# Optimization experiments

Hardware: AMD Instinct MI355X
Metric: run time of the kernel (lower is better)

Reference implementation:

```python
import math
import jax, jax.numpy as jnp
import numpy as np

S = 32.0
M1 = 1.0
M2 = 0.5
M3 = 0.0
MM = M2 * math.sin(math.pi - M2)
NUM_CLASSES = 100000
FEATURES = 512
BATCH = 512


def setup_inputs() -> dict:
    key = jax.random.key(0)
    k1, k2, k3 = jax.random.split(key, 3)
    inputs = jax.random.normal(k1, (BATCH, FEATURES), dtype=jnp.float32)
    labels = jax.random.randint(k2, (BATCH,), 0, NUM_CLASSES, dtype=jnp.int64)
    # xavier_uniform on [num_classes, features]
    limit = math.sqrt(6.0 / (NUM_CLASSES + FEATURES))
    weight = jax.random.uniform(k3, (NUM_CLASSES, FEATURES), minval=-limit, maxval=limit, dtype=jnp.float32)
    return {"inputs": inputs, "labels": labels, "weight": weight}


def reference(inputs, labels, weight):
    # L2 normalize (torch F.normalize uses eps=1e-12 clamp on norm)
    inp_n = inputs / jnp.maximum(jnp.linalg.norm(inputs, axis=1, keepdims=True), 1e-12)
    w_n = weight / jnp.maximum(jnp.linalg.norm(weight, axis=1, keepdims=True), 1e-12)
    cos_in = jnp.clip(inp_n @ w_n.T, -1.0 + 1e-6, 1.0 - 1e-6)  # [N, C]
    theta_in = jnp.arccos(cos_in)
    one_hot = jax.nn.one_hot(labels, NUM_CLASSES, dtype=cos_in.dtype)
    theta_out = theta_in + (theta_in * (M1 - 1.0) + M2) * one_hot
    cos_out = jnp.where(
        theta_out < math.pi,
        jnp.cos(theta_out) - M3 * one_hot,
        cos_in - MM * one_hot - M3 * one_hot,
    )
    outs = S * cos_out  # [N, C]
    # mean cross-entropy
    logp = jax.nn.log_softmax(outs, axis=1)
    n = jnp.arange(BATCH)
    loss = -jnp.mean(logp[n, labels])
    target_cos_in = cos_in[n, labels][:, None]
    target_theta_in = theta_in[n, labels][:, None]
    target_cos_out = cos_out[n, labels][:, None]
    return loss, outs, target_cos_in, target_theta_in, target_cos_out
```

## Files before the change

kernel.cpp:

```cpp
#include <hip/hip_runtime.h>
#include <stdint.h>

#define BATCH 512
#define FEAT 512
#define NCLS 100000
#define BM 128
#define BN 128
#define BK 64
#define NBLK_N 782
#define NBLK (NBLK_N * 4)
#define NCHUNK (NBLK_N * 2)
#define SCALE_S 32.0f
#define MARGIN 0.5f
#define MM_CONST 0.23971276930210156f
#define PI_F 3.14159265358979f

typedef unsigned int u32;
typedef unsigned short u16;
typedef __bf16 bf16x8 __attribute__((ext_vector_type(8)));
typedef float f32x4 __attribute__((ext_vector_type(4)));

__device__ __forceinline__ u16 f2bf(float f) {
  u32 u = __float_as_uint(f);
  u += 0x7fffu + ((u >> 16) & 1u);
  return (u16)(u >> 16);
}

__device__ __forceinline__ void async_copy16(const void* g, void* l) {
  __builtin_amdgcn_global_load_lds((const __attribute__((address_space(1))) u32*)g,
                                   (__attribute__((address_space(3))) u32*)l,
                                   16, 0, 0);
}

__device__ __forceinline__ float block_reduce_sum(float v, float* sbuf) {
  for (int off = 1; off < 64; off <<= 1) v += __shfl_xor(v, off, 64);
  int wid = threadIdx.x >> 6, lane = threadIdx.x & 63;
  __syncthreads();
  if (lane == 0) sbuf[wid] = v;
  __syncthreads();
  return sbuf[0] + sbuf[1] + sbuf[2] + sbuf[3];
}

__global__ __launch_bounds__(256) void norm_all_kernel(const float* __restrict__ inputs,
                                                       const float* __restrict__ weight,
                                                       u16* __restrict__ dstA,
                                                       u16* __restrict__ dstB,
                                                       float* __restrict__ out0) {
  if (blockIdx.x == 0 && threadIdx.x == 0) out0[0] = 0.0f;
  const int lane = threadIdx.x & 63;
  const int gw = (blockIdx.x * 256 + threadIdx.x) >> 6;
  const int nw = gridDim.x * 4;
  for (int row = gw; row < BATCH + NCLS; row += nw) {
    const float* src;
    u16* dst;
    if (row < BATCH) {
      src = inputs + (size_t)row * FEAT;
      dst = dstA + (size_t)row * FEAT;
    } else {
      src = weight + (size_t)(row - BATCH) * FEAT;
      dst = dstB + (size_t)(row - BATCH) * FEAT;
    }
    const float4* p4 = (const float4*)src;
    float4 a = p4[lane];
    float4 b = p4[lane + 64];
    float ss = a.x * a.x + a.y * a.y + a.z * a.z + a.w * a.w +
               b.x * b.x + b.y * b.y + b.z * b.z + b.w * b.w;
#pragma unroll
    for (int off = 1; off < 64; off <<= 1) ss += __shfl_xor(ss, off, 64);
    float inv = 1.0f / fmaxf(sqrtf(ss), 1e-12f);
    ushort4 oa, ob;
    oa.x = f2bf(a.x * inv); oa.y = f2bf(a.y * inv);
    oa.z = f2bf(a.z * inv); oa.w = f2bf(a.w * inv);
    ob.x = f2bf(b.x * inv); ob.y = f2bf(b.y * inv);
    ob.z = f2bf(b.z * inv); ob.w = f2bf(b.w * inv);
    ((ushort4*)dst)[lane] = oa;
    ((ushort4*)dst)[lane + 64] = ob;
  }
}

__global__ __launch_bounds__(256, 3) void gemm_kernel(const u16* __restrict__ A,
                                                      const u16* __restrict__ B,
                                                      const int* __restrict__ labels,
                                                      float* __restrict__ outs,
                                                      float* __restrict__ partials) {
  __shared__ __align__(16) u16 sB0[BN * BK];
  __shared__ __align__(16) u16 sB1[BN * BK];
  __shared__ __align__(16) u16 sB2[BN * BK];
  __shared__ int sLab[BM];

  const int tid = threadIdx.x;
  const int lane = tid & 63;
  const int wid = tid >> 6;
  const int waveM = wid >> 1, waveN = wid & 1;
  const int orig = blockIdx.x;
  const int L = (orig & 7) * (NBLK / 8) + (orig >> 3);
  const int bm = L & 3, bn = L >> 2;
  const int quad = lane >> 4, l15 = lane & 15;

  if (tid < BM) sLab[tid] = labels[bm * BM + tid];

  const u16* gB[4];
#pragma unroll
  for (int rd = 0; rd < 4; ++rd) {
    int idx = rd * 256 + tid;
    int r = idx >> 3;
    int cb = (idx & 7) ^ (r & 7);
    int brow = bn * BN + r;
    if (brow >= NCLS) brow = NCLS - 1;
    gB[rd] = B + (size_t)brow * FEAT + cb * 8;
  }
  const u16* gA = A + (size_t)(bm * BM + waveM * 64 + l15) * FEAT;

  f32x4 acc[4][4] = {};
  bf16x8 a0[4][2], a1[4][2];

#define STAGE_B(SBUF, KT)                                                   \
  do {                                                                      \
    _Pragma("unroll") for (int rd = 0; rd < 4; ++rd)                        \
        async_copy16(gB[rd] + (KT)*BK, &(SBUF)[(rd * 256 + tid) * 8]);      \
  } while (0)

#define LOAD_A(AREG, KT)                                                    \
  do {                                                                      \
    _Pragma("unroll") for (int mi = 0; mi < 4; ++mi)                        \
        _Pragma("unroll") for (int ks = 0; ks < 2; ++ks)                    \
            AREG[mi][ks] = *(const bf16x8*)(gA + (size_t)mi * 16 * FEAT +   \
                                            (KT)*BK + (ks * 4 + quad) * 8); \
  } while (0)

#define COMPUTE(SBUF, AREG)                                                 \
  do {                                                                      \
    _Pragma("unroll") for (int ks = 0; ks < 2; ++ks) {                      \
      int j0 = ks * 4 + quad;                                               \
      bf16x8 bF[4];                                                         \
      _Pragma("unroll") for (int ni = 0; ni < 4; ++ni) {                    \
        int r = waveN * 64 + ni * 16 + l15;                                 \
        bF[ni] = *(const bf16x8*)&(SBUF)[(r * 8 + (j0 ^ (r & 7))) * 8];     \
      }                                                                     \
      _Pragma("unroll") for (int mi = 0; mi < 4; ++mi)                      \
          _Pragma("unroll") for (int ni = 0; ni < 4; ++ni)                  \
              acc[mi][ni] = __builtin_amdgcn_mfma_f32_16x16x32_bf16(        \
                  AREG[mi][ks], bF[ni], acc[mi][ni], 0, 0, 0);              \
    }                                                                       \
  } while (0)

#define SCHED0 __builtin_amdgcn_sched_barrier(0)
#define VMCNT(N) asm volatile("s_waitcnt vmcnt(" #N ")" ::: "memory")
#define BAR asm volatile("s_barrier" ::: "memory")

  STAGE_B(sB0, 0);
  STAGE_B(sB1, 1);
  LOAD_A(a0, 0);
  __syncthreads();

  LOAD_A(a1, 1); SCHED0; STAGE_B(sB2, 2); SCHED0;
  COMPUTE(sB0, a0);
  BAR;
  LOAD_A(a0, 2); SCHED0; STAGE_B(sB0, 3); SCHED0;
  VMCNT(16);
  COMPUTE(sB1, a1);
  BAR;
  LOAD_A(a1, 3); SCHED0; STAGE_B(sB1, 4); SCHED0;
  VMCNT(16); BAR;
  COMPUTE(sB2, a0);
  BAR;
  LOAD_A(a0, 4); SCHED0; STAGE_B(sB2, 5); SCHED0;
  VMCNT(16); BAR;
  COMPUTE(sB0, a1);
  BAR;
  LOAD_A(a1, 5); SCHED0; STAGE_B(sB0, 6); SCHED0;
  VMCNT(16); BAR;
  COMPUTE(sB1, a0);
  BAR;
  LOAD_A(a0, 6); SCHED0; STAGE_B(sB1, 7); SCHED0;
  VMCNT(16); BAR;
  COMPUTE(sB2, a1);
  BAR;
  LOAD_A(a1, 7); SCHED0;
  VMCNT(12); BAR;
  COMPUTE(sB0, a0);
  BAR;
  VMCNT(0); BAR;
  COMPUTE(sB1, a1);

#undef STAGE_B
#undef LOAD_A
#undef COMPUTE

#pragma unroll
  for (int mi = 0; mi < 4; ++mi) {
#pragma unroll
    for (int reg = 0; reg < 4; ++reg) {
      int rloc = waveM * 64 + mi * 16 + quad * 4 + reg;
      int rg = bm * BM + rloc;
      int lab = sLab[rloc];
      float rsum = 0.f;
#pragma unroll
      for (int ni = 0; ni < 4; ++ni) {
        int cg = bn * BN + waveN * 64 + ni * 16 + l15;
        float v = acc[mi][ni][reg];
        v = fminf(fmaxf(v, -1.0f + 1e-6f), 1.0f - 1e-6f);
        if (cg == lab) {
          float th = acosf(v) + MARGIN;
          v = (th < PI_F) ? cosf(th) : (v - MM_CONST);
        }
        v *= SCALE_S;
        if (cg < NCLS) {
          __builtin_nontemporal_store(v, &outs[(size_t)rg * NCLS + cg]);
          rsum += __expf(v - SCALE_S);
        }
      }
#pragma unroll
      for (int off = 1; off < 16; off <<= 1) rsum += __shfl_xor(rsum, off, 64);
      if (l15 == 0) partials[(size_t)rg * NCHUNK + (bn * 2 + waveN)] = rsum;
    }
  }
}

__global__ __launch_bounds__(256) void combine_kernel(const float* __restrict__ partials,
                                                      const float* __restrict__ outs,
                                                      const int* __restrict__ labels,
                                                      const float* __restrict__ inputs,
                                                      const float* __restrict__ weight,
                                                      float* __restrict__ out0,
                                                      float* __restrict__ tdst) {
  __shared__ float sbuf[4];
  int r = blockIdx.x, tid = threadIdx.x;
  int lab = labels[r];

  const float2* px = (const float2*)(inputs + (size_t)r * FEAT);
  const float2* pw = (const float2*)(weight + (size_t)lab * FEAT);
  float2 x = px[tid], w = pw[tid];
  float dot = block_reduce_sum(x.x * w.x + x.y * w.y, sbuf);
  float sx = block_reduce_sum(x.x * x.x + x.y * x.y, sbuf);
  float sw = block_reduce_sum(w.x * w.x + w.y * w.y, sbuf);

  const float* p = partials + (size_t)r * NCHUNK;
  float l = 0.f;
  for (int i = tid; i < NCHUNK; i += 256) l += p[i];
  float lt = block_reduce_sum(l, sbuf);

  if (tid == 0) {
    float lse = SCALE_S + logf(lt);
    float tgt = outs[(size_t)r * NCLS + lab];
    atomicAdd(out0, (lse - tgt) * (1.0f / BATCH));

    float inv = 1.0f / (fmaxf(sqrtf(sx), 1e-12f) * fmaxf(sqrtf(sw), 1e-12f));
    float ci = fminf(fmaxf(dot * inv, -1.0f + 1e-6f), 1.0f - 1e-6f);
    float th = acosf(ci);
    float t2 = th + MARGIN;
    float co = (t2 < PI_F) ? cosf(t2) : (ci - MM_CONST);
    tdst[r] = ci;
    tdst[BATCH + r] = th;
    tdst[2 * BATCH + r] = co;
  }
}

extern "C" void kernel_launch(void* const* d_in, const int* in_sizes, int n_in,
                              void* d_out, int out_size, void* d_ws, size_t ws_size,
                              hipStream_t stream) {
  const float* inputs = (const float*)d_in[0];
  const int* labels = (const int*)d_in[1];
  const float* weight = (const float*)d_in[2];
  float* out = (float*)d_out;
  float* outs = out + 1;
  float* tdst = out + 1 + (size_t)BATCH * NCLS;

  char* ws = (char*)d_ws;
  u16* wsA = (u16*)ws;
  u16* wsB = (u16*)(ws + 524288);
  float* partials = (float*)(ws + 524288 + 102400000);

  norm_all_kernel<<<2048, 256, 0, stream>>>(inputs, weight, wsA, wsB, out);
  gemm_kernel<<<NBLK, 256, 0, stream>>>(wsA, wsB, labels, outs, partials);
  combine_kernel<<<BATCH, 256, 0, stream>>>(partials, outs, labels, inputs, weight, out, tdst);
}
```

Baseline: 563.4 us.

## Load full-K 64-column B tile into LDS once and stream A through registers

```diff
diff --git a/kernel.cpp b/kernel.cpp
--- a/kernel.cpp
+++ b/kernel.cpp
@@ -5,11 +5,10 @@
 #define FEAT 512
 #define NCLS 100000
 #define BM 128
-#define BN 128
-#define BK 64
-#define NBLK_N 782
-#define NBLK (NBLK_N * 4)
-#define NCHUNK (NBLK_N * 2)
+#define BN 64
+#define NBN 1563
+#define NBLK (NBN * 4)
+#define NCHUNK NBN
 #define SCALE_S 32.0f
 #define MARGIN 0.5f
 #define MM_CONST 0.23971276930210156f
@@ -78,126 +77,95 @@
   }
 }
 
-__global__ __launch_bounds__(256, 3) void gemm_kernel(const u16* __restrict__ A,
+__global__ __launch_bounds__(256, 2) void gemm_kernel(const u16* __restrict__ A,
                                                       const u16* __restrict__ B,
                                                       const int* __restrict__ labels,
                                                       float* __restrict__ outs,
                                                       float* __restrict__ partials) {
-  __shared__ __align__(16) u16 sB0[BN * BK];
-  __shared__ __align__(16) u16 sB1[BN * BK];
-  __shared__ __align__(16) u16 sB2[BN * BK];
-  __shared__ int sLab[BM];
+  __shared__ __align__(16) u16 sB[BN * FEAT];
 
   const int tid = threadIdx.x;
   const int lane = tid & 63;
-  const int wid = tid >> 6;
-  const int waveM = wid >> 1, waveN = wid & 1;
-  const int orig = blockIdx.x;
-  const int L = (orig & 7) * (NBLK / 8) + (orig >> 3);
-  const int bm = L & 3, bn = L >> 2;
+  const int w = tid >> 6;
   const int quad = lane >> 4, l15 = lane & 15;
 
-  if (tid < BM) sLab[tid] = labels[bm * BM + tid];
-
-  const u16* gB[4];
-#pragma unroll
-  for (int rd = 0; rd < 4; ++rd) {
-    int idx = rd * 256 + tid;
-    int r = idx >> 3;
-    int cb = (idx & 7) ^ (r & 7);
+  const int o = blockIdx.x;
+  const int xcd = o & 7, slot = o >> 3;
+  const int q = NBLK / 8, rr = NBLK % 8;
+  const int L = (xcd < rr ? xcd * (q + 1) : rr * (q + 1) + (xcd - rr) * q) + slot;
+  const int bn = L >> 2, bm = L & 3;
+
+#pragma unroll
+  for (int p = 0; p < 16; ++p) {
+    int idx = p * 256 + tid;
+    int r = idx >> 6, c = idx & 63;
+    int cg = (c & 56) | ((c & 7) ^ (r & 7));
     int brow = bn * BN + r;
     if (brow >= NCLS) brow = NCLS - 1;
-    gB[rd] = B + (size_t)brow * FEAT + cb * 8;
-  }
-  const u16* gA = A + (size_t)(bm * BM + waveM * 64 + l15) * FEAT;
-
-  f32x4 acc[4][4] = {};
-  bf16x8 a0[4][2], a1[4][2];
-
-#define STAGE_B(SBUF, KT)                                                   \
-  do {                                                                      \
-    _Pragma("unroll") for (int rd = 0; rd < 4; ++rd)                        \
-        async_copy16(gB[rd] + (KT)*BK, &(SBUF)[(rd * 256 + tid) * 8]);      \
+    async_copy16(B + (size_t)brow * FEAT + cg * 8, (u16*)sB + (size_t)idx * 8);
+  }
+  __builtin_amdgcn_sched_barrier(0);
+
+  const u16* gA = A + (size_t)(bm * BM + w * 32 + l15) * FEAT;
+
+  bf16x8 a0[2][2], a1[2][2], a2[2][2];
+
+#define LOAD_A(AR, KT)                                                       \
+  do {                                                                       \
+    _Pragma("unroll") for (int mi = 0; mi < 2; ++mi)                         \
+        _Pragma("unroll") for (int ks = 0; ks < 2; ++ks)                     \
+            AR[mi][ks] = *(const bf16x8*)(gA + (size_t)mi * 16 * FEAT +      \
+                                          (KT)*64 + (ks * 4 + quad) * 8);    \
   } while (0)
 
-#define LOAD_A(AREG, KT)                                                    \
-  do {                                                                      \
-    _Pragma("unroll") for (int mi = 0; mi < 4; ++mi)                        \
-        _Pragma("unroll") for (int ks = 0; ks < 2; ++ks)                    \
-            AREG[mi][ks] = *(const bf16x8*)(gA + (size_t)mi * 16 * FEAT +   \
-                                            (KT)*BK + (ks * 4 + quad) * 8); \
+  LOAD_A(a0, 0);
+  LOAD_A(a1, 1);
+  __builtin_amdgcn_sched_barrier(0);
+  asm volatile("s_waitcnt vmcnt(8)" ::: "memory");
+  asm volatile("s_barrier" ::: "memory");
+  __builtin_amdgcn_sched_barrier(0);
+
+  f32x4 acc[2][4] = {};
+
+#define COMPUTE(AR, KT)                                                      \
+  do {                                                                       \
+    _Pragma("unroll") for (int ks = 0; ks < 2; ++ks) {                       \
+      int j0 = ks * 4 + quad;                                                \
+      bf16x8 bF[4];                                                          \
+      _Pragma("unroll") for (int ni = 0; ni < 4; ++ni) {                     \
+        int r = ni * 16 + l15;                                               \
+        bF[ni] = *(const bf16x8*)&sB[(r * 64 + (KT)*8 + (j0 ^ (r & 7))) * 8];\
+      }                                                                      \
+      _Pragma("unroll") for (int mi = 0; mi < 2; ++mi)                       \
+          _Pragma("unroll") for (int ni = 0; ni < 4; ++ni)                   \
+              acc[mi][ni] = __builtin_amdgcn_mfma_f32_16x16x32_bf16(         \
+                  AR[mi][ks], bF[ni], acc[mi][ni], 0, 0, 0);                 \
+    }                                                                        \
   } while (0)
 
-#define COMPUTE(SBUF, AREG)                                                 \
-  do {                                                                      \
-    _Pragma("unroll") for (int ks = 0; ks < 2; ++ks) {                      \
-      int j0 = ks * 4 + quad;                                               \
-      bf16x8 bF[4];                                                         \
-      _Pragma("unroll") for (int ni = 0; ni < 4; ++ni) {                    \
-        int r = waveN * 64 + ni * 16 + l15;                                 \
-        bF[ni] = *(const bf16x8*)&(SBUF)[(r * 8 + (j0 ^ (r & 7))) * 8];     \
-      }                                                                     \
-      _Pragma("unroll") for (int mi = 0; mi < 4; ++mi)                      \
-          _Pragma("unroll") for (int ni = 0; ni < 4; ++ni)                  \
-              acc[mi][ni] = __builtin_amdgcn_mfma_f32_16x16x32_bf16(        \
-                  AREG[mi][ks], bF[ni], acc[mi][ni], 0, 0, 0);              \
-    }                                                                       \
-  } while (0)
-
-#define SCHED0 __builtin_amdgcn_sched_barrier(0)
-#define VMCNT(N) asm volatile("s_waitcnt vmcnt(" #N ")" ::: "memory")
-#define BAR asm volatile("s_barrier" ::: "memory")
-
-  STAGE_B(sB0, 0);
-  STAGE_B(sB1, 1);
-  LOAD_A(a0, 0);
-  __syncthreads();
-
-  LOAD_A(a1, 1); SCHED0; STAGE_B(sB2, 2); SCHED0;
-  COMPUTE(sB0, a0);
-  BAR;
-  LOAD_A(a0, 2); SCHED0; STAGE_B(sB0, 3); SCHED0;
-  VMCNT(16);
-  COMPUTE(sB1, a1);
-  BAR;
-  LOAD_A(a1, 3); SCHED0; STAGE_B(sB1, 4); SCHED0;
-  VMCNT(16); BAR;
-  COMPUTE(sB2, a0);
-  BAR;
-  LOAD_A(a0, 4); SCHED0; STAGE_B(sB2, 5); SCHED0;
-  VMCNT(16); BAR;
-  COMPUTE(sB0, a1);
-  BAR;
-  LOAD_A(a1, 5); SCHED0; STAGE_B(sB0, 6); SCHED0;
-  VMCNT(16); BAR;
-  COMPUTE(sB1, a0);
-  BAR;
-  LOAD_A(a0, 6); SCHED0; STAGE_B(sB1, 7); SCHED0;
-  VMCNT(16); BAR;
-  COMPUTE(sB2, a1);
-  BAR;
-  LOAD_A(a1, 7); SCHED0;
-  VMCNT(12); BAR;
-  COMPUTE(sB0, a0);
-  BAR;
-  VMCNT(0); BAR;
-  COMPUTE(sB1, a1);
-
-#undef STAGE_B
+  LOAD_A(a2, 2); __builtin_amdgcn_sched_barrier(0); COMPUTE(a0, 0);
+  LOAD_A(a0, 3); __builtin_amdgcn_sched_barrier(0); COMPUTE(a1, 1);
+  LOAD_A(a1, 4); __builtin_amdgcn_sched_barrier(0); COMPUTE(a2, 2);
+  LOAD_A(a2, 5); __builtin_amdgcn_sched_barrier(0); COMPUTE(a0, 3);
+  LOAD_A(a0, 6); __builtin_amdgcn_sched_barrier(0); COMPUTE(a1, 4);
+  LOAD_A(a1, 7); __builtin_amdgcn_sched_barrier(0); COMPUTE(a2, 5);
+  COMPUTE(a0, 6);
+  COMPUTE(a1, 7);
+
 #undef LOAD_A
 #undef COMPUTE
 
 #pragma unroll
-  for (int mi = 0; mi < 4; ++mi) {
+  for (int mi = 0; mi < 2; ++mi) {
 #pragma unroll
     for (int reg = 0; reg < 4; ++reg) {
-      int rloc = waveM * 64 + mi * 16 + quad * 4 + reg;
+      int rloc = w * 32 + mi * 16 + quad * 4 + reg;
       int rg = bm * BM + rloc;
-      int lab = sLab[rloc];
+      int lab = labels[rg];
       float rsum = 0.f;
 #pragma unroll
       for (int ni = 0; ni < 4; ++ni) {
-        int cg = bn * BN + waveN * 64 + ni * 16 + l15;
+        int cg = bn * BN + ni * 16 + l15;
         float v = acc[mi][ni][reg];
         v = fminf(fmaxf(v, -1.0f + 1e-6f), 1.0f - 1e-6f);
         if (cg == lab) {
@@ -206,13 +174,13 @@
         }
         v *= SCALE_S;
         if (cg < NCLS) {
-          __builtin_nontemporal_store(v, &outs[(size_t)rg * NCLS + cg]);
+          outs[(size_t)rg * NCLS + cg] = v;
           rsum += __expf(v - SCALE_S);
         }
       }
 #pragma unroll
       for (int off = 1; off < 16; off <<= 1) rsum += __shfl_xor(rsum, off, 64);
-      if (l15 == 0) partials[(size_t)rg * NCHUNK + (bn * 2 + waveN)] = rsum;
+      if (l15 == 0) partials[(size_t)rg * NCHUNK + bn] = rsum;
     }
   }
 }
```

New measurement: 527.3 us. -6.4%, faster.
